# Performance work log

Measured on AMD Instinct MI355X. Metric: run time of the kernel, lower is better.

Reference implementation:

```python
import jax, jax.numpy as jnp
import numpy as np

STRIDE, PAD, DIL = 1, 1, 1

def _bilinear_sample(inp_flat, py, px, H, W, dtype):
    # inp_flat: [B, C, H*W]; py/px: [B, K, Ho, Wo] float sampling positions
    y0 = jnp.floor(py); x0 = jnp.floor(px)
    ly = py - y0; lx = px - x0
    y0i = y0.astype(jnp.int32); x0i = x0.astype(jnp.int32)

    def gather(yi, xi):
        valid = (yi >= 0) & (yi < H) & (xi >= 0) & (xi < W)
        idx = jnp.clip(yi, 0, H - 1) * W + jnp.clip(xi, 0, W - 1)  # [B,K,Ho,Wo]
        vals = jax.vmap(lambda xf, ix: xf[:, ix])(inp_flat, idx)    # [B,C,K,Ho,Wo]
        return vals * valid[:, None].astype(dtype)

    out = ((1 - ly) * (1 - lx))[:, None] * gather(y0i, x0i)
    out = out + ((1 - ly) * lx)[:, None] * gather(y0i, x0i + 1)
    out = out + (ly * (1 - lx))[:, None] * gather(y0i + 1, x0i)
    out = out + (ly * lx)[:, None] * gather(y0i + 1, x0i + 1)
    return out  # [B, C, K, Ho, Wo]

def setup_inputs() -> dict:
    key = jax.random.key(0)
    k1, k2, k3, k4 = jax.random.split(key, 4)
    B, Cin, Cout, H, W, kh, kw = 8, 128, 128, 64, 64, 3, 3
    n = Cin * kh * kw
    stdv = 1.0 / np.sqrt(n)
    inp = jax.random.normal(k1, (B, Cin, H, W), dtype=jnp.float32)
    offset = jax.random.normal(k2, (B, 2 * kh * kw, H, W), dtype=jnp.float32)
    mask = jax.random.uniform(k3, (B, kh * kw, H, W), dtype=jnp.float32)
    weight = jax.random.uniform(k4, (Cout, Cin, kh, kw), dtype=jnp.float32,
                                minval=-stdv, maxval=stdv)
    bias = jnp.zeros((Cout,), dtype=jnp.float32)
    return {"input": inp, "offset": offset, "mask": mask, "weight": weight, "bias": bias}

def reference(input, offset, mask, weight, bias):
    B, C, H, W = input.shape
    Cout, Cin, kh, kw = weight.shape
    K = kh * kw
    Ho = (H + 2 * PAD - DIL * (kh - 1) - 1) // STRIDE + 1
    Wo = (W + 2 * PAD - DIL * (kw - 1) - 1) // STRIDE + 1
    dtype = input.dtype

    # Offset channel layout (DCNv2): channel 2k = dy, 2k+1 = dx for kernel tap k
    off_y = offset[:, 0::2]  # [B, K, Ho, Wo]
    off_x = offset[:, 1::2]

    ky, kx = jnp.meshgrid(jnp.arange(kh), jnp.arange(kw), indexing="ij")
    ky = (ky.reshape(-1) * DIL).astype(dtype)  # [K]
    kx = (kx.reshape(-1) * DIL).astype(dtype)
    base_y = (jnp.arange(Ho) * STRIDE - PAD).astype(dtype)  # [Ho]
    base_x = (jnp.arange(Wo) * STRIDE - PAD).astype(dtype)

    py = off_y + base_y[None, None, :, None] + ky[None, :, None, None]  # [B,K,Ho,Wo]
    px = off_x + base_x[None, None, None, :] + kx[None, :, None, None]

    inp_flat = input.reshape(B, C, H * W)
    sampled = _bilinear_sample(inp_flat, py, px, H, W, dtype)  # [B,C,K,Ho,Wo]
    cols = sampled * mask[:, None]                              # modulation

    w2 = weight.reshape(Cout, Cin * K)
    cols2 = cols.reshape(B, Cin * K, Ho * Wo)
    out = jnp.einsum("om,bmp->bop", w2, cols2).reshape(B, Cout, Ho, Wo)
    return out + bias[None, :, None, None]
```

## Files before the change

### kernel.cpp

```cpp
#include <hip/hip_runtime.h>


constexpr int CIN = 128, COUT = 128, H = 64, W = 64, KK = 9;
constexpr int HW = H * W;
constexpr int SROW = 136;

typedef __attribute__((ext_vector_type(8))) short short8;
typedef __attribute__((ext_vector_type(4))) float float4v;

static __device__ __forceinline__ unsigned short f32_to_bf16_rne(float f) {
  unsigned u = __float_as_uint(f);
  return (unsigned short)((u + 0x7FFFu + ((u >> 16) & 1u)) >> 16);
}
static __device__ __forceinline__ float blo(unsigned u) {
  return __uint_as_float(u << 16);
}
static __device__ __forceinline__ float bhi(unsigned u) {
  return __uint_as_float(u & 0xFFFF0000u);
}

__global__ __launch_bounds__(256) void tprep_kernel(
    const float* __restrict__ in, unsigned short* __restrict__ inT) {
  __shared__ unsigned short lt[64 * 130];
  const int b = blockIdx.x >> 6, y = blockIdx.x & 63;
  for (int i = threadIdx.x; i < 128 * 64; i += 256) {
    const int ci = i >> 6, x = i & 63;
    lt[x * 130 + ci] = f32_to_bf16_rne(in[((b * 128 + ci) * 64 + y) * 64 + x]);
  }
  __syncthreads();
  unsigned* outp = (unsigned*)inT + (size_t)(b * 64 + y) * 64 * 64;
  for (int i = threadIdx.x; i < 64 * 64; i += 256) {
    const int x = i >> 6, c2 = (i & 63) * 2;
    outp[x * 64 + (i & 63)] =
        (unsigned)lt[x * 130 + c2] | ((unsigned)lt[x * 130 + c2 + 1] << 16);
  }
}

__global__ __launch_bounds__(256) void wprep_kernel(
    const float* __restrict__ w, unsigned short* __restrict__ wt) {
  const int t = blockIdx.x * 256 + threadIdx.x;
  if (t >= 9 * 4 * 8 * 64) return;
  const int lane = t & 63, c16 = (t >> 6) & 7, kt = t >> 9;
  const int ks = kt & 3, k = kt >> 2;
  const int co = c16 * 16 + (lane & 15);
  const int ci0 = ks * 32 + (lane >> 4) * 8;
  unsigned pk[4];
#pragma unroll
  for (int jj = 0; jj < 4; ++jj) {
    const unsigned short h0 =
        f32_to_bf16_rne(w[(co * CIN + ci0 + 2 * jj) * KK + k]);
    const unsigned short h1 =
        f32_to_bf16_rne(w[(co * CIN + ci0 + 2 * jj + 1) * KK + k]);
    pk[jj] = (unsigned)h0 | ((unsigned)h1 << 16);
  }
  *(uint4*)(wt + (size_t)t * 8) = make_uint4(pk[0], pk[1], pk[2], pk[3]);
}

__global__ __launch_bounds__(512, 8) void dcn_mfma_kernel(
    const unsigned short* __restrict__ inT, const float* __restrict__ offset,
    const float* __restrict__ mask, const unsigned short* __restrict__ wt,
    const float* __restrict__ bias, float* __restrict__ out) {
  __shared__ int2 pos_i[KK * 32];
  __shared__ float4 pos_w[KK * 32];
  __shared__ unsigned short s_t[2][32 * SROW];

  const int b = blockIdx.x & 7;
  const int ho = (blockIdx.x >> 3) & 63;
  const int ph = blockIdx.x >> 9;
  const int tid = threadIdx.x;

  if (tid < KK * 32) {
    const int k = tid >> 5, p = tid & 31;
    const int pg = ph * 32 + p;
    const int ky = k / 3, kx = k - 3 * ky;
    const float py = (float)(ho - 1 + ky) +
                     offset[((b * 18 + 2 * k) * 64 + ho) * 64 + pg];
    const float px = (float)(pg - 1 + kx) +
                     offset[((b * 18 + 2 * k + 1) * 64 + ho) * 64 + pg];
    const float m = mask[((b * 9 + k) * 64 + ho) * 64 + pg];
    const float y0f = floorf(py), x0f = floorf(px);
    const int y0 = (int)y0f, x0 = (int)x0f;
    const float ly = py - y0f, lx = px - x0f;
    const float hy = 1.f - ly, hx = 1.f - lx;
    const bool vy0 = (y0 >= 0) && (y0 < H);
    const bool vy1 = (y0 + 1 >= 0) && (y0 + 1 < H);
    const bool vx0 = (x0 >= 0) && (x0 < W);
    const bool vx1 = (x0 + 1 >= 0) && (x0 + 1 < W);
    const float w00 = (vy0 && vx0) ? hy * hx * m : 0.f;
    const float w01 = (vy0 && vx1) ? hy * lx * m : 0.f;
    const float w10 = (vy1 && vx0) ? ly * hx * m : 0.f;
    const float w11 = (vy1 && vx1) ? ly * lx * m : 0.f;
    const int cy0 = min(max(y0, 0), H - 1), cy1 = min(max(y0 + 1, 0), H - 1);
    const int bx = min(max(x0, 0), W - 2);
    const int s0 = min(max(x0 - bx, 0), 1);
    const int s1 = min(max(x0 + 1 - bx, 0), 1);
    const float cA0 = (s0 == 0 ? w00 : 0.f) + (s1 == 0 ? w01 : 0.f);
    const float cB0 = (s0 == 1 ? w00 : 0.f) + (s1 == 1 ? w01 : 0.f);
    const float cA1 = (s0 == 0 ? w10 : 0.f) + (s1 == 0 ? w11 : 0.f);
    const float cB1 = (s0 == 1 ? w10 : 0.f) + (s1 == 1 ? w11 : 0.f);
    pos_i[tid] = make_int2((cy0 * 64 + bx) * 128, (cy1 * 64 + bx) * 128);
    pos_w[tid] = make_float4(cA0, cB0, cA1, cB1);
  }
  __syncthreads();

  const int wave = tid >> 6;
  const int lane = tid & 63;
  const int quad = lane >> 4, l15 = lane & 15;
  const int p_loc = tid >> 4;
  const int cg = tid & 15;

  float4v acc0 = (float4v)(0.f), acc1 = (float4v)(0.f);

  const unsigned short* inb = inT + (size_t)b * HW * 128;

  int2 P = pos_i[p_loc];
  float4 Wc = pos_w[p_loc];
  uint4 g00, g01, g10, g11;
  {
    const unsigned short* a0 = inb + P.x + cg * 8;
    const unsigned short* a1 = inb + P.y + cg * 8;
    g00 = *(const uint4*)a0;
    g01 = *(const uint4*)(a0 + 128);
    g10 = *(const uint4*)a1;
    g11 = *(const uint4*)(a1 + 128);
  }

  for (int k = 0; k < KK; ++k) {
    const int buf = k & 1;
    {
      const unsigned u00[4] = {g00.x, g00.y, g00.z, g00.w};
      const unsigned u01[4] = {g01.x, g01.y, g01.z, g01.w};
      const unsigned u10[4] = {g10.x, g10.y, g10.z, g10.w};
      const unsigned u11[4] = {g11.x, g11.y, g11.z, g11.w};
      unsigned pk[4];
#pragma unroll
      for (int j = 0; j < 4; ++j) {
        const float se = Wc.x * blo(u00[j]) + Wc.y * blo(u01[j]) +
                         Wc.z * blo(u10[j]) + Wc.w * blo(u11[j]);
        const float so = Wc.x * bhi(u00[j]) + Wc.y * bhi(u01[j]) +
                         Wc.z * bhi(u10[j]) + Wc.w * bhi(u11[j]);
        pk[j] = (unsigned)f32_to_bf16_rne(se) |
                ((unsigned)f32_to_bf16_rne(so) << 16);
      }
      *(uint4*)&s_t[buf][p_loc * SROW + cg * 8] =
          make_uint4(pk[0], pk[1], pk[2], pk[3]);
    }
    __syncthreads();

    short8 A0, A1, A2, A3;
    {
      const unsigned short* wk =
          wt + ((size_t)(k * 4) * 8 + wave) * 512 + (size_t)lane * 8;
      A0 = *(const short8*)(wk);
      A1 = *(const short8*)(wk + 8 * 512);
      A2 = *(const short8*)(wk + 16 * 512);
      A3 = *(const short8*)(wk + 24 * 512);
    }

    if (k < KK - 1) {
      P = pos_i[(k + 1) * 32 + p_loc];
      Wc = pos_w[(k + 1) * 32 + p_loc];
      const unsigned short* a0 = inb + P.x + cg * 8;
      const unsigned short* a1 = inb + P.y + cg * 8;
      g00 = *(const uint4*)a0;
      g01 = *(const uint4*)(a0 + 128);
      g10 = *(const uint4*)a1;
      g11 = *(const uint4*)(a1 + 128);
    }

#pragma unroll
    for (int ks = 0; ks < 4; ++ks) {
      const int col = ks * 32 + quad * 8;
      const short8 b0 = *(const short8*)&s_t[buf][l15 * SROW + col];
      const short8 b1 = *(const short8*)&s_t[buf][(16 + l15) * SROW + col];
      const short8 Ak = (ks == 0) ? A0 : (ks == 1) ? A1 : (ks == 2) ? A2 : A3;
      acc0 = __builtin_amdgcn_mfma_f32_16x16x32_bf16(Ak, b0, acc0, 0, 0, 0);
      acc1 = __builtin_amdgcn_mfma_f32_16x16x32_bf16(Ak, b1, acc1, 0, 0, 0);
    }
  }

#pragma unroll
  for (int r = 0; r < 4; ++r) {
    const int co = wave * 16 + quad * 4 + r;
    const float bb = bias[co];
    float* op = out + ((size_t)(b * COUT + co) * H + ho) * W + ph * 32;
    op[l15] = acc0[r] + bb;
    op[16 + l15] = acc1[r] + bb;
  }
}

__global__ __launch_bounds__(256) void dcn_fp32_kernel(
    const float* __restrict__ input, const float* __restrict__ offset,
    const float* __restrict__ mask, const float* __restrict__ weight,
    const float* __restrict__ bias, float* __restrict__ out) {
  __shared__ short4 pos_o[KK * 64];
  __shared__ float4 pos_w[KK * 64];
  __shared__ float s_tile[64 * 64];
  __shared__ float w_tile[64 * 128];
  const int b = blockIdx.x >> 6;
  const int ho = blockIdx.x & 63;
  const int tid = threadIdx.x;
  for (int idx = tid; idx < KK * 64; idx += 256) {
    const int k = idx >> 6, pp = idx & 63;
    const int ky = k / 3, kx = k - 3 * ky;
    const float py = (float)(ho - 1 + ky) +
                     offset[((b * 18 + 2 * k) * 64 + ho) * 64 + pp];
    const float px = (float)(pp - 1 + kx) +
                     offset[((b * 18 + 2 * k + 1) * 64 + ho) * 64 + pp];
    const float m = mask[((b * 9 + k) * 64 + ho) * 64 + pp];
    const float y0f = floorf(py), x0f = floorf(px);
    const int y0 = (int)y0f, x0 = (int)x0f;
    const float ly = py - y0f, lx = px - x0f;
    const float hy = 1.f - ly, hx = 1.f - lx;
    const bool vy0 = (y0 >= 0) && (y0 < H), vy1 = (y0 + 1 >= 0) && (y0 + 1 < H);
    const bool vx0 = (x0 >= 0) && (x0 < W), vx1 = (x0 + 1 >= 0) && (x0 + 1 < W);
    const int cy0 = min(max(y0, 0), H - 1), cy1 = min(max(y0 + 1, 0), H - 1);
    const int cx0 = min(max(x0, 0), W - 1), cx1 = min(max(x0 + 1, 0), W - 1);
    pos_o[idx] = make_short4((short)(cy0 * W + cx0), (short)(cy0 * W + cx1),
                             (short)(cy1 * W + cx0), (short)(cy1 * W + cx1));
    pos_w[idx] = make_float4((vy0 && vx0) ? hy * hx * m : 0.f,
                             (vy0 && vx1) ? hy * lx * m : 0.f,
                             (vy1 && vx0) ? ly * hx * m : 0.f,
                             (vy1 && vx1) ? ly * lx * m : 0.f);
  }
  const int cog = tid >> 4, pg = tid & 15;
  float acc[8][4];
#pragma unroll
  for (int j = 0; j < 8; ++j)
#pragma unroll
    for (int q = 0; q < 4; ++q) acc[j][q] = 0.f;
  const float* inp_b = input + (size_t)b * CIN * HW;
  for (int k = 0; k < KK; ++k) {
    for (int cc = 0; cc < 2; ++cc) {
      __syncthreads();
      for (int i = tid; i < 64 * 64; i += 256) {
        const int cil = i >> 6, pp = i & 63;
        const float* plane = inp_b + (size_t)(cc * 64 + cil) * HW;
        const short4 o = pos_o[k * 64 + pp];
        const float4 w = pos_w[k * 64 + pp];
        s_tile[i] = w.x * plane[(int)o.x] + w.y * plane[(int)o.y] +
                    w.z * plane[(int)o.z] + w.w * plane[(int)o.w];
      }
      for (int i = tid; i < 64 * 128; i += 256) {
        const int cil = i & 63, co = i >> 6;
        w_tile[cil * 128 + co] = weight[(co * CIN + cc * 64 + cil) * KK + k];
      }
      __syncthreads();
#pragma unroll 8
      for (int cil = 0; cil < 64; ++cil) {
        const float4 sv = *(const float4*)&s_tile[cil * 64 + (pg << 2)];
        const float4 wa = *(const float4*)&w_tile[cil * 128 + (cog << 3)];
        const float4 wb = *(const float4*)&w_tile[cil * 128 + (cog << 3) + 4];
        const float s4[4] = {sv.x, sv.y, sv.z, sv.w};
        const float w8[8] = {wa.x, wa.y, wa.z, wa.w, wb.x, wb.y, wb.z, wb.w};
#pragma unroll
        for (int j = 0; j < 8; ++j)
#pragma unroll
          for (int q = 0; q < 4; ++q) acc[j][q] = fmaf(w8[j], s4[q], acc[j][q]);
      }
    }
  }
  float* outp = out + (size_t)b * COUT * HW + ho * W;
#pragma unroll
  for (int j = 0; j < 8; ++j) {
    const int co = (cog << 3) + j;
    const float bb = bias[co];
    *(float4*)&outp[co * HW + (pg << 2)] =
        make_float4(acc[j][0] + bb, acc[j][1] + bb, acc[j][2] + bb,
                    acc[j][3] + bb);
  }
}

extern "C" void kernel_launch(void* const* d_in, const int* in_sizes, int n_in,
                              void* d_out, int out_size, void* d_ws,
                              size_t ws_size, hipStream_t stream) {
  const float* input = (const float*)d_in[0];
  const float* offset = (const float*)d_in[1];
  const float* mask = (const float*)d_in[2];
  const float* weight = (const float*)d_in[3];
  const float* bias = (const float*)d_in[4];
  float* out = (float*)d_out;

  const size_t wt_bytes = (size_t)9 * 4 * 8 * 64 * 8 * 2;
  const size_t inT_bytes = (size_t)8 * HW * 128 * 2;
  if (ws_size >= wt_bytes + inT_bytes) {
    unsigned short* wt = (unsigned short*)d_ws;
    unsigned short* inT = (unsigned short*)((char*)d_ws + wt_bytes);
    hipLaunchKernelGGL(wprep_kernel, dim3(72), dim3(256), 0, stream, weight, wt);
    hipLaunchKernelGGL(tprep_kernel, dim3(512), dim3(256), 0, stream, input, inT);
    hipLaunchKernelGGL(dcn_mfma_kernel, dim3(1024), dim3(512), 0, stream, inT,
                       offset, mask, wt, bias, out);
  } else {
    hipLaunchKernelGGL(dcn_fp32_kernel, dim3(512), dim3(256), 0, stream, input,
                       offset, mask, weight, bias, out);
  }
}
```

Baseline: 105.9 us.

## Halve block size, give each wave two output-channel tiles, XOR-swizzle LDS

The MFMA kernel now runs 256 threads per block instead of 512. Each wave computes 32 output channels (two 16-row A tiles) against the same B fragments, so every LDS B read feeds four MFMAs instead of two. Each thread now gathers and blends 16 channels per sample position instead of 8. The padded LDS row stride is replaced by an XOR swizzle to avoid bank conflicts. This raises per-thread register use and loads in flight, and the launch bound asks for fewer blocks per CU.

New measurement: 107.4 us. No clear change (+1.4%).

```diff
diff --git a/kernel.cpp b/kernel.cpp
--- a/kernel.cpp
+++ b/kernel.cpp
@@ -3,7 +3,6 @@
 
 constexpr int CIN = 128, COUT = 128, H = 64, W = 64, KK = 9;
 constexpr int HW = H * W;
-constexpr int SROW = 136;
 
 typedef __attribute__((ext_vector_type(8))) short short8;
 typedef __attribute__((ext_vector_type(4))) float float4v;
@@ -56,21 +55,21 @@
   *(uint4*)(wt + (size_t)t * 8) = make_uint4(pk[0], pk[1], pk[2], pk[3]);
 }
 
-__global__ __launch_bounds__(512, 8) void dcn_mfma_kernel(
+__global__ __launch_bounds__(256, 4) void dcn_mfma_kernel(
     const unsigned short* __restrict__ inT, const float* __restrict__ offset,
     const float* __restrict__ mask, const unsigned short* __restrict__ wt,
     const float* __restrict__ bias, float* __restrict__ out) {
   __shared__ int2 pos_i[KK * 32];
   __shared__ float4 pos_w[KK * 32];
-  __shared__ unsigned short s_t[2][32 * SROW];
+  __shared__ unsigned short s_t[2][32 * 128];
 
   const int b = blockIdx.x & 7;
   const int ho = (blockIdx.x >> 3) & 63;
   const int ph = blockIdx.x >> 9;
   const int tid = threadIdx.x;
 
-  if (tid < KK * 32) {
-    const int k = tid >> 5, p = tid & 31;
+  for (int idx = tid; idx < KK * 32; idx += 256) {
+    const int k = idx >> 5, p = idx & 31;
     const int pg = ph * 32 + p;
     const int ky = k / 3, kx = k - 3 * ky;
     const float py = (float)(ho - 1 + ky) +
@@ -98,94 +97,124 @@
     const float cB0 = (s0 == 1 ? w00 : 0.f) + (s1 == 1 ? w01 : 0.f);
     const float cA1 = (s0 == 0 ? w10 : 0.f) + (s1 == 0 ? w11 : 0.f);
     const float cB1 = (s0 == 1 ? w10 : 0.f) + (s1 == 1 ? w11 : 0.f);
-    pos_i[tid] = make_int2((cy0 * 64 + bx) * 128, (cy1 * 64 + bx) * 128);
-    pos_w[tid] = make_float4(cA0, cB0, cA1, cB1);
+    pos_i[idx] = make_int2((cy0 * 64 + bx) * 128, (cy1 * 64 + bx) * 128);
+    pos_w[idx] = make_float4(cA0, cB0, cA1, cB1);
   }
   __syncthreads();
 
   const int wave = tid >> 6;
   const int lane = tid & 63;
   const int quad = lane >> 4, l15 = lane & 15;
-  const int p_loc = tid >> 4;
-  const int cg = tid & 15;
-
-  float4v acc0 = (float4v)(0.f), acc1 = (float4v)(0.f);
+  const int p_loc = tid >> 3;
+  const int cg8 = tid & 7;
+
+  float4v acc[2][2];
+#pragma unroll
+  for (int s = 0; s < 2; ++s)
+#pragma unroll
+    for (int n = 0; n < 2; ++n) acc[s][n] = (float4v)(0.f);
 
   const unsigned short* inb = inT + (size_t)b * HW * 128;
 
   int2 P = pos_i[p_loc];
   float4 Wc = pos_w[p_loc];
-  uint4 g00, g01, g10, g11;
+  uint4 ga0, ga1, gb0, gb1, gc0, gc1, gd0, gd1;
   {
-    const unsigned short* a0 = inb + P.x + cg * 8;
-    const unsigned short* a1 = inb + P.y + cg * 8;
-    g00 = *(const uint4*)a0;
-    g01 = *(const uint4*)(a0 + 128);
-    g10 = *(const uint4*)a1;
-    g11 = *(const uint4*)(a1 + 128);
+    const unsigned short* a0 = inb + P.x + cg8 * 16;
+    const unsigned short* a1 = inb + P.y + cg8 * 16;
+    ga0 = *(const uint4*)a0;
+    ga1 = *(const uint4*)(a0 + 8);
+    gb0 = *(const uint4*)(a0 + 128);
+    gb1 = *(const uint4*)(a0 + 136);
+    gc0 = *(const uint4*)a1;
+    gc1 = *(const uint4*)(a1 + 8);
+    gd0 = *(const uint4*)(a1 + 128);
+    gd1 = *(const uint4*)(a1 + 136);
   }
 
   for (int k = 0; k < KK; ++k) {
     const int buf = k & 1;
     {
-      const unsigned u00[4] = {g00.x, g00.y, g00.z, g00.w};
-      const unsigned u01[4] = {g01.x, g01.y, g01.z, g01.w};
-      const unsigned u10[4] = {g10.x, g10.y, g10.z, g10.w};
-      const unsigned u11[4] = {g11.x, g11.y, g11.z, g11.w};
-      unsigned pk[4];
-#pragma unroll
-      for (int j = 0; j < 4; ++j) {
-        const float se = Wc.x * blo(u00[j]) + Wc.y * blo(u01[j]) +
-                         Wc.z * blo(u10[j]) + Wc.w * blo(u11[j]);
-        const float so = Wc.x * bhi(u00[j]) + Wc.y * bhi(u01[j]) +
-                         Wc.z * bhi(u10[j]) + Wc.w * bhi(u11[j]);
-        pk[j] = (unsigned)f32_to_bf16_rne(se) |
-                ((unsigned)f32_to_bf16_rne(so) << 16);
-      }
-      *(uint4*)&s_t[buf][p_loc * SROW + cg * 8] =
-          make_uint4(pk[0], pk[1], pk[2], pk[3]);
+      const uint4 A4[2] = {ga0, ga1}, B4[2] = {gb0, gb1};
+      const uint4 C4[2] = {gc0, gc1}, D4[2] = {gd0, gd1};
+#pragma unroll
+      for (int h = 0; h < 2; ++h) {
+        const unsigned u00[4] = {A4[h].x, A4[h].y, A4[h].z, A4[h].w};
+        const unsigned u01[4] = {B4[h].x, B4[h].y, B4[h].z, B4[h].w};
+        const unsigned u10[4] = {C4[h].x, C4[h].y, C4[h].z, C4[h].w};
+        const unsigned u11[4] = {D4[h].x, D4[h].y, D4[h].z, D4[h].w};
+        unsigned pk[4];
+#pragma unroll
+        for (int j = 0; j < 4; ++j) {
+          const float se = Wc.x * blo(u00[j]) + Wc.y * blo(u01[j]) +
+                           Wc.z * blo(u10[j]) + Wc.w * blo(u11[j]);
+          const float so = Wc.x * bhi(u00[j]) + Wc.y * bhi(u01[j]) +
+                           Wc.z * bhi(u10[j]) + Wc.w * bhi(u11[j]);
+          pk[j] = (unsigned)f32_to_bf16_rne(se) |
+                  ((unsigned)f32_to_bf16_rne(so) << 16);
+        }
+        const int gi = cg8 * 2 + h;
+        const int pgr = gi ^ (p_loc & 7);
+        *(uint4*)&s_t[buf][p_loc * 128 + pgr * 8] =
+            make_uint4(pk[0], pk[1], pk[2], pk[3]);
+      }
     }
     __syncthreads();
 
-    short8 A0, A1, A2, A3;
+    short8 A[4][2];
     {
       const unsigned short* wk =
-          wt + ((size_t)(k * 4) * 8 + wave) * 512 + (size_t)lane * 8;
-      A0 = *(const short8*)(wk);
-      A1 = *(const short8*)(wk + 8 * 512);
-      A2 = *(const short8*)(wk + 16 * 512);
-      A3 = *(const short8*)(wk + 24 * 512);
+          wt + ((size_t)(k * 4) * 8 + wave * 2) * 512 + (size_t)lane * 8;
+#pragma unroll
+      for (int ks = 0; ks < 4; ++ks) {
+        A[ks][0] = *(const short8*)(wk + (size_t)ks * 8 * 512);
+        A[ks][1] = *(const short8*)(wk + (size_t)ks * 8 * 512 + 512);
+      }
     }
 
     if (k < KK - 1) {
       P = pos_i[(k + 1) * 32 + p_loc];
       Wc = pos_w[(k + 1) * 32 + p_loc];
-      const unsigned short* a0 = inb + P.x + cg * 8;
-      const unsigned short* a1 = inb + P.y + cg * 8;
-      g00 = *(const uint4*)a0;
-      g01 = *(const uint4*)(a0 + 128);
-      g10 = *(const uint4*)a1;
-      g11 = *(const uint4*)(a1 + 128);
+      const unsigned short* a0 = inb + P.x + cg8 * 16;
+      const unsigned short* a1 = inb + P.y + cg8 * 16;
+      ga0 = *(const uint4*)a0;
+      ga1 = *(const uint4*)(a0 + 8);
+      gb0 = *(const uint4*)(a0 + 128);
+      gb1 = *(const uint4*)(a0 + 136);
+      gc0 = *(const uint4*)a1;
+      gc1 = *(const uint4*)(a1 + 8);
+      gd0 = *(const uint4*)(a1 + 128);
+      gd1 = *(const uint4*)(a1 + 136);
     }
 
 #pragma unroll
     for (int ks = 0; ks < 4; ++ks) {
-      const int col = ks * 32 + quad * 8;
-      const short8 b0 = *(const short8*)&s_t[buf][l15 * SROW + col];
-      const short8 b1 = *(const short8*)&s_t[buf][(16 + l15) * SROW + col];
-      const short8 Ak = (ks == 0) ? A0 : (ks == 1) ? A1 : (ks == 2) ? A2 : A3;
-      acc0 = __builtin_amdgcn_mfma_f32_16x16x32_bf16(Ak, b0, acc0, 0, 0, 0);
-      acc1 = __builtin_amdgcn_mfma_f32_16x16x32_bf16(Ak, b1, acc1, 0, 0, 0);
-    }
-  }
-
-#pragma unroll
-  for (int r = 0; r < 4; ++r) {
-    const int co = wave * 16 + quad * 4 + r;
-    const float bb = bias[co];
-    float* op = out + ((size_t)(b * COUT + co) * H + ho) * W + ph * 32;
-    op[l15] = acc0[r] + bb;
-    op[16 + l15] = acc1[r] + bb;
+      const int gi = ks * 4 + quad;
+      const int o0 = l15 * 128 + (gi ^ (l15 & 7)) * 8;
+      const int o1 = (16 + l15) * 128 + (gi ^ (l15 & 7)) * 8;
+      const short8 b0 = *(const short8*)&s_t[buf][o0];
+      const short8 b1 = *(const short8*)&s_t[buf][o1];
+      acc[0][0] =
+          __builtin_amdgcn_mfma_f32_16x16x32_bf16(A[ks][0], b0, acc[0][0], 0, 0, 0);
+      acc[0][1] =
+          __builtin_amdgcn_mfma_f32_16x16x32_bf16(A[ks][0], b1, acc[0][1], 0, 0, 0);
+      acc[1][0] =
+          __builtin_amdgcn_mfma_f32_16x16x32_bf16(A[ks][1], b0, acc[1][0], 0, 0, 0);
+      acc[1][1] =
+          __builtin_amdgcn_mfma_f32_16x16x32_bf16(A[ks][1], b1, acc[1][1], 0, 0, 0);
+    }
+  }
+
+#pragma unroll
+  for (int sub = 0; sub < 2; ++sub) {
+#pragma unroll
+    for (int r = 0; r < 4; ++r) {
+      const int co = wave * 32 + sub * 16 + quad * 4 + r;
+      const float bb = bias[co];
+      float* op = out + ((size_t)(b * COUT + co) * H + ho) * W + ph * 32;
+      op[l15] = acc[sub][0][r] + bb;
+      op[16 + l15] = acc[sub][1][r] + bb;
+    }
   }
 }
 
@@ -288,7 +317,7 @@
     unsigned short* inT = (unsigned short*)((char*)d_ws + wt_bytes);
     hipLaunchKernelGGL(wprep_kernel, dim3(72), dim3(256), 0, stream, weight, wt);
     hipLaunchKernelGGL(tprep_kernel, dim3(512), dim3(256), 0, stream, input, inT);
-    hipLaunchKernelGGL(dcn_mfma_kernel, dim3(1024), dim3(512), 0, stream, inT,
+    hipLaunchKernelGGL(dcn_mfma_kernel, dim3(1024), dim3(256), 0, stream, inT,
                        offset, mask, wt, bias, out);
   } else {
     hipLaunchKernelGGL(dcn_fp32_kernel, dim3(512), dim3(256), 0, stream, input,
```

## Split MFMA reduction dimension across waves and sample directly into registers

Applied to the files above, without the earlier changes.

Changes the main kernel from splitting output channels across 8 waves to splitting the input-channel (K) dimension across 4 waves. Each wave bilinearly samples its own 32-channel slice straight into MFMA B-operand registers and computes all 128 output channels, which removes the shared-memory staging tile and the per-tap block barrier. The partial sums are then combined through a two-stage shared-memory reduction before wave 0 writes the output. The cost is 64 accumulator registers per lane, the weight-fragment loads held in registers, lower occupancy (256 threads, 3 blocks per unit), a larger LDS reduction buffer, and removal of the software prefetch of the next tap's gathers.

Result: slower. 134.2 us (+26.7%).

```diff
diff --git a/kernel.cpp b/kernel.cpp
--- a/kernel.cpp
+++ b/kernel.cpp
@@ -3,7 +3,7 @@
 
 constexpr int CIN = 128, COUT = 128, H = 64, W = 64, KK = 9;
 constexpr int HW = H * W;
-constexpr int SROW = 136;
+constexpr int RST = 33;
 
 typedef __attribute__((ext_vector_type(8))) short short8;
 typedef __attribute__((ext_vector_type(4))) float float4v;
@@ -17,6 +17,25 @@
 }
 static __device__ __forceinline__ float bhi(unsigned u) {
   return __uint_as_float(u & 0xFFFF0000u);
+}
+static __device__ __forceinline__ unsigned pkdw(unsigned u00, unsigned u01,
+                                                unsigned u10, unsigned u11,
+                                                float4 Wc) {
+  const float se = Wc.x * blo(u00) + Wc.y * blo(u01) + Wc.z * blo(u10) +
+                   Wc.w * blo(u11);
+  const float so = Wc.x * bhi(u00) + Wc.y * bhi(u01) + Wc.z * bhi(u10) +
+                   Wc.w * bhi(u11);
+  return (unsigned)f32_to_bf16_rne(se) | ((unsigned)f32_to_bf16_rne(so) << 16);
+}
+static __device__ __forceinline__ short8 bilerp8(uint4 t00, uint4 t01,
+                                                 uint4 t10, uint4 t11,
+                                                 float4 Wc) {
+  union { uint4 u; short8 s; } r;
+  r.u = make_uint4(pkdw(t00.x, t01.x, t10.x, t11.x, Wc),
+                   pkdw(t00.y, t01.y, t10.y, t11.y, Wc),
+                   pkdw(t00.z, t01.z, t10.z, t11.z, Wc),
+                   pkdw(t00.w, t01.w, t10.w, t11.w, Wc));
+  return r.s;
 }
 
 __global__ __launch_bounds__(256) void tprep_kernel(
@@ -56,21 +75,22 @@
   *(uint4*)(wt + (size_t)t * 8) = make_uint4(pk[0], pk[1], pk[2], pk[3]);
 }
 
-__global__ __launch_bounds__(512, 8) void dcn_mfma_kernel(
+__global__ __launch_bounds__(256, 3) void dcn_mfma_kernel(
     const unsigned short* __restrict__ inT, const float* __restrict__ offset,
     const float* __restrict__ mask, const unsigned short* __restrict__ wt,
     const float* __restrict__ bias, float* __restrict__ out) {
   __shared__ int2 pos_i[KK * 32];
   __shared__ float4 pos_w[KK * 32];
-  __shared__ unsigned short s_t[2][32 * SROW];
+  __shared__ float red0[128 * RST];
+  __shared__ float red1[128 * RST];
 
   const int b = blockIdx.x & 7;
   const int ho = (blockIdx.x >> 3) & 63;
   const int ph = blockIdx.x >> 9;
   const int tid = threadIdx.x;
 
-  if (tid < KK * 32) {
-    const int k = tid >> 5, p = tid & 31;
+  for (int idx = tid; idx < KK * 32; idx += 256) {
+    const int k = idx >> 5, p = idx & 31;
     const int pg = ph * 32 + p;
     const int ky = k / 3, kx = k - 3 * ky;
     const float py = (float)(ho - 1 + ky) +
@@ -98,94 +118,123 @@
     const float cB0 = (s0 == 1 ? w00 : 0.f) + (s1 == 1 ? w01 : 0.f);
     const float cA1 = (s0 == 0 ? w10 : 0.f) + (s1 == 0 ? w11 : 0.f);
     const float cB1 = (s0 == 1 ? w10 : 0.f) + (s1 == 1 ? w11 : 0.f);
-    pos_i[tid] = make_int2((cy0 * 64 + bx) * 128, (cy1 * 64 + bx) * 128);
-    pos_w[tid] = make_float4(cA0, cB0, cA1, cB1);
+    pos_i[idx] = make_int2((cy0 * 64 + bx) * 128, (cy1 * 64 + bx) * 128);
+    pos_w[idx] = make_float4(cA0, cB0, cA1, cB1);
   }
   __syncthreads();
 
   const int wave = tid >> 6;
   const int lane = tid & 63;
   const int quad = lane >> 4, l15 = lane & 15;
-  const int p_loc = tid >> 4;
-  const int cg = tid & 15;
-
-  float4v acc0 = (float4v)(0.f), acc1 = (float4v)(0.f);
+  const int ciofs = wave * 32 + quad * 8;
+
+  float4v acc[8][2];
+#pragma unroll
+  for (int s = 0; s < 8; ++s)
+#pragma unroll
+    for (int n = 0; n < 2; ++n) acc[s][n] = (float4v)(0.f);
 
   const unsigned short* inb = inT + (size_t)b * HW * 128;
 
-  int2 P = pos_i[p_loc];
-  float4 Wc = pos_w[p_loc];
-  uint4 g00, g01, g10, g11;
-  {
-    const unsigned short* a0 = inb + P.x + cg * 8;
-    const unsigned short* a1 = inb + P.y + cg * 8;
-    g00 = *(const uint4*)a0;
-    g01 = *(const uint4*)(a0 + 128);
-    g10 = *(const uint4*)a1;
-    g11 = *(const uint4*)(a1 + 128);
-  }
-
   for (int k = 0; k < KK; ++k) {
-    const int buf = k & 1;
-    {
-      const unsigned u00[4] = {g00.x, g00.y, g00.z, g00.w};
-      const unsigned u01[4] = {g01.x, g01.y, g01.z, g01.w};
-      const unsigned u10[4] = {g10.x, g10.y, g10.z, g10.w};
-      const unsigned u11[4] = {g11.x, g11.y, g11.z, g11.w};
-      unsigned pk[4];
-#pragma unroll
-      for (int j = 0; j < 4; ++j) {
-        const float se = Wc.x * blo(u00[j]) + Wc.y * blo(u01[j]) +
-                         Wc.z * blo(u10[j]) + Wc.w * blo(u11[j]);
-        const float so = Wc.x * bhi(u00[j]) + Wc.y * bhi(u01[j]) +
-                         Wc.z * bhi(u10[j]) + Wc.w * bhi(u11[j]);
-        pk[j] = (unsigned)f32_to_bf16_rne(se) |
-                ((unsigned)f32_to_bf16_rne(so) << 16);
+    const int2 P0 = pos_i[k * 32 + l15];
+    const float4 W0 = pos_w[k * 32 + l15];
+    const int2 P1 = pos_i[k * 32 + 16 + l15];
+    const float4 W1 = pos_w[k * 32 + 16 + l15];
+    const unsigned short* r00 = inb + P0.x + ciofs;
+    const unsigned short* r01 = inb + P0.y + ciofs;
+    const unsigned short* r10 = inb + P1.x + ciofs;
+    const unsigned short* r11 = inb + P1.y + ciofs;
+    const uint4 t0a = *(const uint4*)r00;
+    const uint4 t0b = *(const uint4*)(r00 + 128);
+    const uint4 t0c = *(const uint4*)r01;
+    const uint4 t0d = *(const uint4*)(r01 + 128);
+    const uint4 t1a = *(const uint4*)r10;
+    const uint4 t1b = *(const uint4*)(r10 + 128);
+    const uint4 t1c = *(const uint4*)r11;
+    const uint4 t1d = *(const uint4*)(r11 + 128);
+    const unsigned short* wk =
+        wt + ((size_t)(k * 4 + wave) * 8) * 512 + (size_t)lane * 8;
+    short8 A[8];
+#pragma unroll
+    for (int sub = 0; sub < 8; ++sub)
+      A[sub] = *(const short8*)(wk + (size_t)sub * 512);
+    const short8 B0 = bilerp8(t0a, t0b, t0c, t0d, W0);
+    const short8 B1 = bilerp8(t1a, t1b, t1c, t1d, W1);
+#pragma unroll
+    for (int sub = 0; sub < 8; ++sub) {
+      acc[sub][0] =
+          __builtin_amdgcn_mfma_f32_16x16x32_bf16(A[sub], B0, acc[sub][0], 0, 0, 0);
+      acc[sub][1] =
+          __builtin_amdgcn_mfma_f32_16x16x32_bf16(A[sub], B1, acc[sub][1], 0, 0, 0);
+    }
+  }
+
+  if (wave == 2) {
+#pragma unroll
+    for (int sub = 0; sub < 8; ++sub)
+#pragma unroll
+      for (int ns = 0; ns < 2; ++ns)
+#pragma unroll
+        for (int r = 0; r < 4; ++r)
+          red0[(sub * 16 + quad * 4 + r) * RST + ns * 16 + l15] =
+              acc[sub][ns][r];
+  } else if (wave == 3) {
+#pragma unroll
+    for (int sub = 0; sub < 8; ++sub)
+#pragma unroll
+      for (int ns = 0; ns < 2; ++ns)
+#pragma unroll
+        for (int r = 0; r < 4; ++r)
+          red1[(sub * 16 + quad * 4 + r) * RST + ns * 16 + l15] =
+              acc[sub][ns][r];
+  }
+  __syncthreads();
+  if (wave == 0) {
+#pragma unroll
+    for (int sub = 0; sub < 8; ++sub)
+#pragma unroll
+      for (int ns = 0; ns < 2; ++ns)
+#pragma unroll
+        for (int r = 0; r < 4; ++r)
+          acc[sub][ns][r] +=
+              red0[(sub * 16 + quad * 4 + r) * RST + ns * 16 + l15];
+  } else if (wave == 1) {
+#pragma unroll
+    for (int sub = 0; sub < 8; ++sub)
+#pragma unroll
+      for (int ns = 0; ns < 2; ++ns)
+#pragma unroll
+        for (int r = 0; r < 4; ++r)
+          acc[sub][ns][r] +=
+              red1[(sub * 16 + quad * 4 + r) * RST + ns * 16 + l15];
+  }
+  __syncthreads();
+  if (wave == 1) {
+#pragma unroll
+    for (int sub = 0; sub < 8; ++sub)
+#pragma unroll
+      for (int ns = 0; ns < 2; ++ns)
+#pragma unroll
+        for (int r = 0; r < 4; ++r)
+          red0[(sub * 16 + quad * 4 + r) * RST + ns * 16 + l15] =
+              acc[sub][ns][r];
+  }
+  __syncthreads();
+  if (wave == 0) {
+#pragma unroll
+    for (int sub = 0; sub < 8; ++sub) {
+#pragma unroll
+      for (int r = 0; r < 4; ++r) {
+        const int co = sub * 16 + quad * 4 + r;
+        const float bb = bias[co];
+        float* op = out + ((size_t)(b * COUT + co) * H + ho) * W + ph * 32;
+#pragma unroll
+        for (int ns = 0; ns < 2; ++ns)
+          op[ns * 16 + l15] =
+              acc[sub][ns][r] + red0[co * RST + ns * 16 + l15] + bb;
       }
-      *(uint4*)&s_t[buf][p_loc * SROW + cg * 8] =
-          make_uint4(pk[0], pk[1], pk[2], pk[3]);
     }
-    __syncthreads();
-
-    short8 A0, A1, A2, A3;
-    {
-      const unsigned short* wk =
-          wt + ((size_t)(k * 4) * 8 + wave) * 512 + (size_t)lane * 8;
-      A0 = *(const short8*)(wk);
-      A1 = *(const short8*)(wk + 8 * 512);
-      A2 = *(const short8*)(wk + 16 * 512);
-      A3 = *(const short8*)(wk + 24 * 512);
-    }
-
-    if (k < KK - 1) {
-      P = pos_i[(k + 1) * 32 + p_loc];
-      Wc = pos_w[(k + 1) * 32 + p_loc];
-      const unsigned short* a0 = inb + P.x + cg * 8;
-      const unsigned short* a1 = inb + P.y + cg * 8;
-      g00 = *(const uint4*)a0;
-      g01 = *(const uint4*)(a0 + 128);
-      g10 = *(const uint4*)a1;
-      g11 = *(const uint4*)(a1 + 128);
-    }
-
-#pragma unroll
-    for (int ks = 0; ks < 4; ++ks) {
-      const int col = ks * 32 + quad * 8;
-      const short8 b0 = *(const short8*)&s_t[buf][l15 * SROW + col];
-      const short8 b1 = *(const short8*)&s_t[buf][(16 + l15) * SROW + col];
-      const short8 Ak = (ks == 0) ? A0 : (ks == 1) ? A1 : (ks == 2) ? A2 : A3;
-      acc0 = __builtin_amdgcn_mfma_f32_16x16x32_bf16(Ak, b0, acc0, 0, 0, 0);
-      acc1 = __builtin_amdgcn_mfma_f32_16x16x32_bf16(Ak, b1, acc1, 0, 0, 0);
-    }
-  }
-
-#pragma unroll
-  for (int r = 0; r < 4; ++r) {
-    const int co = wave * 16 + quad * 4 + r;
-    const float bb = bias[co];
-    float* op = out + ((size_t)(b * COUT + co) * H + ho) * W + ph * 32;
-    op[l15] = acc0[r] + bb;
-    op[16 + l15] = acc1[r] + bb;
   }
 }
 
@@ -288,7 +337,7 @@
     unsigned short* inT = (unsigned short*)((char*)d_ws + wt_bytes);
     hipLaunchKernelGGL(wprep_kernel, dim3(72), dim3(256), 0, stream, weight, wt);
     hipLaunchKernelGGL(tprep_kernel, dim3(512), dim3(256), 0, stream, input, inT);
-    hipLaunchKernelGGL(dcn_mfma_kernel, dim3(1024), dim3(512), 0, stream, inT,
+    hipLaunchKernelGGL(dcn_mfma_kernel, dim3(1024), dim3(256), 0, stream, inT,
                        offset, mask, wt, bias, out);
   } else {
     hipLaunchKernelGGL(dcn_fp32_kernel, dim3(512), dim3(256), 0, stream, input,
```
